# Kernel tuning notes

Measured on AMD Instinct MI355X. Metric: run time of the kernel, lower is better.

## Reference

```python
import jax, jax.numpy as jnp
import numpy as np
from jax import lax

B, S, T = 2048, 4096, 3


def setup_inputs() -> dict:
    key = jax.random.key(0)
    k_em, k_tr, k_st, k_en, k_tg = jax.random.split(key, 5)
    emissions = jax.random.normal(k_em, (B, S, T), dtype=jnp.float32)
    # reset_parameters(): uniform(-0.1, 0.1)
    transitions = jax.random.uniform(k_tr, (T, T), minval=-0.1, maxval=0.1, dtype=jnp.float32)
    start_transitions = jax.random.uniform(k_st, (T,), minval=-0.1, maxval=0.1, dtype=jnp.float32)
    end_transitions = jax.random.uniform(k_en, (T,), minval=-0.1, maxval=0.1, dtype=jnp.float32)
    tags = jax.random.randint(k_tg, (B, S), 0, T, dtype=jnp.int32)
    mask = jnp.ones((B, S), dtype=jnp.int32)
    return {
        "emissions": emissions,
        "transitions": transitions,
        "start_transitions": start_transitions,
        "end_transitions": end_transitions,
        "tags": tags,
        "mask": mask,
    }


def _crf_nll(emissions, transitions, start_transitions, end_transitions, tags, mask):
    # batch_first=True -> transpose to time-major (S, B, ...)
    em = jnp.transpose(emissions, (1, 0, 2))  # (S, B, T)
    tg = jnp.transpose(tags, (1, 0))          # (S, B)
    mk = jnp.transpose(mask, (1, 0))          # (S, B)
    batch_idx = jnp.arange(em.shape[1])

    # ---- log partition (forward algorithm) ----
    alpha0 = start_transitions[None, :] + em[0]  # (B, T)

    def fwd_step(alpha, inp):
        e, m = inp  # e: (B,T), m: (B,)
        # alpha[b,i] + trans[i,j] + e[b,j] -> logsumexp over i
        nxt = jax.nn.logsumexp(alpha[:, :, None] + transitions[None, :, :] + e[:, None, :], axis=1)
        alpha = jnp.where((m > 0)[:, None], nxt, alpha)
        return alpha, None

    alpha, _ = lax.scan(fwd_step, alpha0, (em[1:], mk[1:]))
    log_partition = jax.nn.logsumexp(alpha + end_transitions[None, :], axis=1)  # (B,)

    # ---- gold score ----
    score0 = start_transitions[tg[0]] + em[0][batch_idx, tg[0]]  # (B,)

    def score_step(carry, inp):
        score, prev = carry
        e, t, m = inp
        add = transitions[prev, t] + e[batch_idx, t]
        score = score + jnp.where(m > 0, add, jnp.zeros_like(score))
        return (score, t), None

    (score, _), _ = lax.scan(score_step, (score0, tg[0]), (em[1:], tg[1:], mk[1:]))
    seq_lens = jnp.sum(mk, axis=0)  # (B,)
    last_tags = tg[seq_lens - 1, batch_idx]
    score = score + end_transitions[last_tags]

    return jnp.mean(log_partition - score)


def reference(emissions, transitions, start_transitions, end_transitions, tags, mask):
    return _crf_nll(emissions, transitions, start_transitions, end_transitions, tags, mask)
```

## Files before the change

kernel.cpp:

```cpp
#include <hip/hip_runtime.h>
#include <math.h>

#define CRF_B 2048
#define CRF_S 4096
#define LN2F  0.6931471805599453f

__device__ __forceinline__ float fexp2(float x) { return __builtin_amdgcn_exp2f(x); }

#define CRF_MERGE(aq0,aq1,aq2,aq3,aq4,aq5,aq6,aq7,aq8,aC0,aC1,aC2,asc,acn, \
                  bq0,bq1,bq2,bq3,bq4,bq5,bq6,bq7,bq8,bC0,bC1,bC2,bsc,bcn) { \
    int cm_ = max(max(bC0,bC1),bC2);                                        \
    int d0_=bC0-cm_, d1_=bC1-cm_, d2_=bC2-cm_;                              \
    float s0_ = (d0_>-127)? __int_as_float((127+d0_)<<23) : 0.f;            \
    float s1_ = (d1_>-127)? __int_as_float((127+d1_)<<23) : 0.f;            \
    float s2_ = (d2_>-127)? __int_as_float((127+d2_)<<23) : 0.f;            \
    float b0_=bq0*s0_, b1_=bq1*s0_, b2_=bq2*s0_;                            \
    float b3_=bq3*s1_, b4_=bq4*s1_, b5_=bq5*s1_;                            \
    float b6_=bq6*s2_, b7_=bq7*s2_, b8_=bq8*s2_;                            \
    float r0_=aq0*b0_+aq1*b3_+aq2*b6_;                                      \
    float r1_=aq0*b1_+aq1*b4_+aq2*b7_;                                      \
    float r2_=aq0*b2_+aq1*b5_+aq2*b8_;                                      \
    float r3_=aq3*b0_+aq4*b3_+aq5*b6_;                                      \
    float r4_=aq3*b1_+aq4*b4_+aq5*b7_;                                      \
    float r5_=aq3*b2_+aq4*b5_+aq5*b8_;                                      \
    float r6_=aq6*b0_+aq7*b3_+aq8*b6_;                                      \
    float r7_=aq6*b1_+aq7*b4_+aq8*b7_;                                      \
    float r8_=aq6*b2_+aq7*b5_+aq8*b8_;                                      \
    float mx_; int ex_; float sc_;                                          \
    mx_=fmaxf(fmaxf(r0_,r1_),r2_); ex_=((__float_as_int(mx_)>>23)&255)-127; \
    sc_=__int_as_float((127-ex_)<<23);                                      \
    aq0=r0_*sc_; aq1=r1_*sc_; aq2=r2_*sc_; aC0=aC0+cm_+ex_;                 \
    mx_=fmaxf(fmaxf(r3_,r4_),r5_); ex_=((__float_as_int(mx_)>>23)&255)-127; \
    sc_=__int_as_float((127-ex_)<<23);                                      \
    aq3=r3_*sc_; aq4=r4_*sc_; aq5=r5_*sc_; aC1=aC1+cm_+ex_;                 \
    mx_=fmaxf(fmaxf(r6_,r7_),r8_); ex_=((__float_as_int(mx_)>>23)&255)-127; \
    sc_=__int_as_float((127-ex_)<<23);                                      \
    aq6=r6_*sc_; aq7=r7_*sc_; aq8=r8_*sc_; aC2=aC2+cm_+ex_;                 \
    asc += bsc; acn += bcn; }

__global__ __launch_bounds__(512, 6) void crf_row_kernel(
    const float* __restrict__ em,
    const float* __restrict__ trans,
    const float* __restrict__ startt,
    const float* __restrict__ endt,
    const int*   __restrict__ tags,
    const int*   __restrict__ mask,
    float* __restrict__ perb)
{
    __shared__ float s_tr[9];
    __shared__ float s_rq[8][10];
    __shared__ int   s_rc[8][4];

    const int tid = threadIdx.x;
    const int w = tid >> 6, l = tid & 63;
    const int b = blockIdx.x;
    const long cbase = (long)b * CRF_S + (long)tid * 8;

    if (tid < 9) s_tr[tid] = trans[tid];
    __syncthreads();

    const float4* e4 = (const float4*)(em + cbase * 3);
    float4 ev0 = e4[0], ev1 = e4[1], ev2 = e4[2],
           ev3 = e4[3], ev4 = e4[4], ev5 = e4[5];
    const int4* t4 = (const int4*)(tags + cbase);
    int4 ta = t4[0], tb = t4[1];
    const int4* m4 = (const int4*)(mask + cbase);
    int4 ma = m4[0], mb = m4[1];
    int p = 0;
    if (tid > 0) p = tags[cbase - 1];

    float e[24] = { ev0.x, ev0.y, ev0.z, ev0.w, ev1.x, ev1.y, ev1.z, ev1.w,
                    ev2.x, ev2.y, ev2.z, ev2.w, ev3.x, ev3.y, ev3.z, ev3.w,
                    ev4.x, ev4.y, ev4.z, ev4.w, ev5.x, ev5.y, ev5.z, ev5.w };
    unsigned ttag =  (unsigned)(ta.x & 3)        | ((unsigned)(ta.y & 3) << 2)
                  | ((unsigned)(ta.z & 3) << 4)  | ((unsigned)(ta.w & 3) << 6)
                  | ((unsigned)(tb.x & 3) << 8)  | ((unsigned)(tb.y & 3) << 10)
                  | ((unsigned)(tb.z & 3) << 12) | ((unsigned)(tb.w & 3) << 14);
    unsigned tmsk =  (unsigned)(ma.x != 0)       | ((unsigned)(ma.y != 0) << 1)
                  | ((unsigned)(ma.z != 0) << 2) | ((unsigned)(ma.w != 0) << 3)
                  | ((unsigned)(mb.x != 0) << 4) | ((unsigned)(mb.y != 0) << 5)
                  | ((unsigned)(mb.z != 0) << 6) | ((unsigned)(mb.w != 0) << 7);

    float Etr[9];
    #pragma unroll
    for (int k = 0; k < 9; ++k) Etr[k] = __expf(s_tr[k]);

    float q0=1.f,q1=0.f,q2=0.f, q3=0.f,q4=1.f,q5=0.f, q6=0.f,q7=0.f,q8=1.f;
    int C0=0, C1=0, C2=0;
    float score = 0.f; int cnt = 0;

    #pragma unroll
    for (int t = 0; t < 8; ++t) {
        float e0 = e[3*t], e1 = e[3*t+1], e2 = e[3*t+2];
        int tv = (int)((ttag >> (2*t)) & 3u);
        int mv = (int)((tmsk >> t) & 1u);
        if (mv && !((t == 0) && (tid == 0))) {
            float X0 = __expf(e0), X1 = __expf(e1), X2 = __expf(e2);
            float n0, n1, n2;
            n0 = q0*Etr[0] + q1*Etr[3] + q2*Etr[6];
            n1 = q0*Etr[1] + q1*Etr[4] + q2*Etr[7];
            n2 = q0*Etr[2] + q1*Etr[5] + q2*Etr[8];
            q0 = n0*X0; q1 = n1*X1; q2 = n2*X2;
            n0 = q3*Etr[0] + q4*Etr[3] + q5*Etr[6];
            n1 = q3*Etr[1] + q4*Etr[4] + q5*Etr[7];
            n2 = q3*Etr[2] + q4*Etr[5] + q5*Etr[8];
            q3 = n0*X0; q4 = n1*X1; q5 = n2*X2;
            n0 = q6*Etr[0] + q7*Etr[3] + q8*Etr[6];
            n1 = q6*Etr[1] + q7*Etr[4] + q8*Etr[7];
            n2 = q6*Etr[2] + q7*Etr[5] + q8*Etr[8];
            q6 = n0*X0; q7 = n1*X1; q8 = n2*X2;
            float ev = (tv == 0) ? e0 : (tv == 1) ? e1 : e2;
            score += s_tr[p * 3 + tv] + ev;
            ++cnt;
        }
        p = tv;
        if ((t & 3) == 3) {
            float mx; int ex; float sc;
            mx = fmaxf(fmaxf(q0, q1), q2);
            ex = ((__float_as_int(mx) >> 23) & 255) - 127;
            sc = __int_as_float((127 - ex) << 23);
            q0 *= sc; q1 *= sc; q2 *= sc; C0 += ex;
            mx = fmaxf(fmaxf(q3, q4), q5);
            ex = ((__float_as_int(mx) >> 23) & 255) - 127;
            sc = __int_as_float((127 - ex) << 23);
            q3 *= sc; q4 *= sc; q5 *= sc; C1 += ex;
            mx = fmaxf(fmaxf(q6, q7), q8);
            ex = ((__float_as_int(mx) >> 23) & 255) - 127;
            sc = __int_as_float((127 - ex) << 23);
            q6 *= sc; q7 *= sc; q8 *= sc; C2 += ex;
        }
    }

    #pragma unroll
    for (int st = 1; st < 64; st <<= 1) {
        float nq0 = __shfl_down(q0, st), nq1 = __shfl_down(q1, st),
              nq2 = __shfl_down(q2, st), nq3 = __shfl_down(q3, st),
              nq4 = __shfl_down(q4, st), nq5 = __shfl_down(q5, st),
              nq6 = __shfl_down(q6, st), nq7 = __shfl_down(q7, st),
              nq8 = __shfl_down(q8, st);
        int nC0 = __shfl_down(C0, st), nC1 = __shfl_down(C1, st),
            nC2 = __shfl_down(C2, st);
        float nsc = __shfl_down(score, st);
        int   ncn = __shfl_down(cnt, st);
        CRF_MERGE(q0,q1,q2,q3,q4,q5,q6,q7,q8,C0,C1,C2,score,cnt,
                  nq0,nq1,nq2,nq3,nq4,nq5,nq6,nq7,nq8,nC0,nC1,nC2,nsc,ncn);
    }

    if (l == 0) {
        s_rq[w][0]=q0; s_rq[w][1]=q1; s_rq[w][2]=q2;
        s_rq[w][3]=q3; s_rq[w][4]=q4; s_rq[w][5]=q5;
        s_rq[w][6]=q6; s_rq[w][7]=q7; s_rq[w][8]=q8;
        s_rq[w][9]=score;
        s_rc[w][0]=C0; s_rc[w][1]=C1; s_rc[w][2]=C2; s_rc[w][3]=cnt;
    }
    __syncthreads();

    if (tid == 0) {
        float a0=s_rq[0][0], a1=s_rq[0][1], a2=s_rq[0][2],
              a3=s_rq[0][3], a4=s_rq[0][4], a5=s_rq[0][5],
              a6=s_rq[0][6], a7=s_rq[0][7], a8=s_rq[0][8];
        float asc = s_rq[0][9];
        int AC0=s_rc[0][0], AC1=s_rc[0][1], AC2=s_rc[0][2], acn=s_rc[0][3];
        #pragma unroll
        for (int w2 = 1; w2 < 8; ++w2) {
            float m0=s_rq[w2][0], m1=s_rq[w2][1], m2=s_rq[w2][2],
                  m3=s_rq[w2][3], m4=s_rq[w2][4], m5=s_rq[w2][5],
                  m6=s_rq[w2][6], m7=s_rq[w2][7], m8=s_rq[w2][8];
            float msc = s_rq[w2][9];
            int mc0=s_rc[w2][0], mc1=s_rc[w2][1], mc2=s_rc[w2][2], mcn=s_rc[w2][3];
            CRF_MERGE(a0,a1,a2,a3,a4,a5,a6,a7,a8,AC0,AC1,AC2,asc,acn,
                      m0,m1,m2,m3,m4,m5,m6,m7,m8,mc0,mc1,mc2,msc,mcn);
        }
        int tg0 = (int)(ttag & 3u), mk0 = (int)(tmsk & 1u);
        float la0 = startt[0] + e[0];
        float la1 = startt[1] + e[1];
        float la2 = startt[2] + e[2];
        float am = fmaxf(fmaxf(la0, la1), la2);
        int cm = max(max(AC0, AC1), AC2);
        float w0 = __expf(la0 - am) * fexp2((float)(AC0 - cm));
        float w1 = __expf(la1 - am) * fexp2((float)(AC1 - cm));
        float w2v = __expf(la2 - am) * fexp2((float)(AC2 - cm));
        float v0 = w0*a0 + w1*a3 + w2v*a6;
        float v1 = w0*a1 + w1*a4 + w2v*a7;
        float v2 = w0*a2 + w1*a5 + w2v*a8;
        float sum = v0 * __expf(endt[0]) + v1 * __expf(endt[1])
                  + v2 * __expf(endt[2]);
        float lp = am + (float)cm * LN2F + __logf(sum);

        float sc = asc + startt[tg0]
                 + ((tg0 == 0) ? e[0] : (tg0 == 1) ? e[1] : e[2]);
        int cn = acn + mk0;
        int lastidx = (cn > 0) ? (cn - 1) : 0;
        sc += endt[tags[(long)b * CRF_S + lastidx]];

        perb[b] = lp - sc;
    }
}

__global__ __launch_bounds__(256) void crf_reduce_kernel(
    const float* __restrict__ perb, float* __restrict__ out)
{
    __shared__ float sdata[256];
    const int tid = threadIdx.x;
    float s = 0.f;
    for (int i = tid; i < CRF_B; i += 256) s += perb[i];
    sdata[tid] = s;
    __syncthreads();
    for (int off = 128; off > 0; off >>= 1) {
        if (tid < off) sdata[tid] += sdata[tid + off];
        __syncthreads();
    }
    if (tid == 0) out[0] = sdata[0] * (1.0f / (float)CRF_B);
}

extern "C" void kernel_launch(void* const* d_in, const int* in_sizes, int n_in,
                              void* d_out, int out_size, void* d_ws, size_t ws_size,
                              hipStream_t stream)
{
    const float* em     = (const float*)d_in[0];
    const float* trans  = (const float*)d_in[1];
    const float* startt = (const float*)d_in[2];
    const float* endt   = (const float*)d_in[3];
    const int*   tags   = (const int*)d_in[4];
    const int*   mask   = (const int*)d_in[5];
    float* out = (float*)d_out;

    float* perb = (float*)d_ws;

    crf_row_kernel<<<CRF_B, 512, 0, stream>>>(
        em, trans, startt, endt, tags, mask, perb);
    crf_reduce_kernel<<<1, 256, 0, stream>>>(perb, out);
}
```

Baseline: 45.10 us.

## Use single shared scale exponent per matrix and double per-thread sequence chunk

Each thread now processes 16 timesteps instead of 8 with 256-thread blocks, halving the depth of the cross-wave merge work. The per-row exponent tracking of the 3x3 transfer matrices is collapsed into one shared scale exponent per matrix, which simplifies the merge macro (no per-row rescale) and the final combine. Thread 0 also reuses its own registers instead of rereading shared memory. The single exponent risks underflow of small rows when row magnitudes diverge, though with small transitions this is benign; higher register use may reduce occupancy.

Measured after the change: 59.11 us. 31.1% more time.

```diff
diff --git a/kernel.cpp b/kernel.cpp
--- a/kernel.cpp
+++ b/kernel.cpp
@@ -5,40 +5,29 @@
 #define CRF_S 4096
 #define LN2F  0.6931471805599453f
 
-__device__ __forceinline__ float fexp2(float x) { return __builtin_amdgcn_exp2f(x); }
-
-#define CRF_MERGE(aq0,aq1,aq2,aq3,aq4,aq5,aq6,aq7,aq8,aC0,aC1,aC2,asc,acn, \
-                  bq0,bq1,bq2,bq3,bq4,bq5,bq6,bq7,bq8,bC0,bC1,bC2,bsc,bcn) { \
-    int cm_ = max(max(bC0,bC1),bC2);                                        \
-    int d0_=bC0-cm_, d1_=bC1-cm_, d2_=bC2-cm_;                              \
-    float s0_ = (d0_>-127)? __int_as_float((127+d0_)<<23) : 0.f;            \
-    float s1_ = (d1_>-127)? __int_as_float((127+d1_)<<23) : 0.f;            \
-    float s2_ = (d2_>-127)? __int_as_float((127+d2_)<<23) : 0.f;            \
-    float b0_=bq0*s0_, b1_=bq1*s0_, b2_=bq2*s0_;                            \
-    float b3_=bq3*s1_, b4_=bq4*s1_, b5_=bq5*s1_;                            \
-    float b6_=bq6*s2_, b7_=bq7*s2_, b8_=bq8*s2_;                            \
-    float r0_=aq0*b0_+aq1*b3_+aq2*b6_;                                      \
-    float r1_=aq0*b1_+aq1*b4_+aq2*b7_;                                      \
-    float r2_=aq0*b2_+aq1*b5_+aq2*b8_;                                      \
-    float r3_=aq3*b0_+aq4*b3_+aq5*b6_;                                      \
-    float r4_=aq3*b1_+aq4*b4_+aq5*b7_;                                      \
-    float r5_=aq3*b2_+aq4*b5_+aq5*b8_;                                      \
-    float r6_=aq6*b0_+aq7*b3_+aq8*b6_;                                      \
-    float r7_=aq6*b1_+aq7*b4_+aq8*b7_;                                      \
-    float r8_=aq6*b2_+aq7*b5_+aq8*b8_;                                      \
-    float mx_; int ex_; float sc_;                                          \
-    mx_=fmaxf(fmaxf(r0_,r1_),r2_); ex_=((__float_as_int(mx_)>>23)&255)-127; \
-    sc_=__int_as_float((127-ex_)<<23);                                      \
-    aq0=r0_*sc_; aq1=r1_*sc_; aq2=r2_*sc_; aC0=aC0+cm_+ex_;                 \
-    mx_=fmaxf(fmaxf(r3_,r4_),r5_); ex_=((__float_as_int(mx_)>>23)&255)-127; \
-    sc_=__int_as_float((127-ex_)<<23);                                      \
-    aq3=r3_*sc_; aq4=r4_*sc_; aq5=r5_*sc_; aC1=aC1+cm_+ex_;                 \
-    mx_=fmaxf(fmaxf(r6_,r7_),r8_); ex_=((__float_as_int(mx_)>>23)&255)-127; \
-    sc_=__int_as_float((127-ex_)<<23);                                      \
-    aq6=r6_*sc_; aq7=r7_*sc_; aq8=r8_*sc_; aC2=aC2+cm_+ex_;                 \
+#define CRF_MERGE(aq0,aq1,aq2,aq3,aq4,aq5,aq6,aq7,aq8,aC,asc,acn, \
+                  bq0,bq1,bq2,bq3,bq4,bq5,bq6,bq7,bq8,bC,bsc,bcn) { \
+    float r0_=aq0*bq0+aq1*bq3+aq2*bq6;                              \
+    float r1_=aq0*bq1+aq1*bq4+aq2*bq7;                              \
+    float r2_=aq0*bq2+aq1*bq5+aq2*bq8;                              \
+    float r3_=aq3*bq0+aq4*bq3+aq5*bq6;                              \
+    float r4_=aq3*bq1+aq4*bq4+aq5*bq7;                              \
+    float r5_=aq3*bq2+aq4*bq5+aq5*bq8;                              \
+    float r6_=aq6*bq0+aq7*bq3+aq8*bq6;                              \
+    float r7_=aq6*bq1+aq7*bq4+aq8*bq7;                              \
+    float r8_=aq6*bq2+aq7*bq5+aq8*bq8;                              \
+    float mx_ = fmaxf(fmaxf(fmaxf(fmaxf(r0_,r1_),r2_),              \
+                            fmaxf(fmaxf(r3_,r4_),r5_)),             \
+                      fmaxf(fmaxf(r6_,r7_),r8_));                   \
+    int ex_ = ((__float_as_int(mx_)>>23)&255)-127;                  \
+    float sc_ = __int_as_float((127-ex_)<<23);                      \
+    aq0=r0_*sc_; aq1=r1_*sc_; aq2=r2_*sc_;                          \
+    aq3=r3_*sc_; aq4=r4_*sc_; aq5=r5_*sc_;                          \
+    aq6=r6_*sc_; aq7=r7_*sc_; aq8=r8_*sc_;                          \
+    aC = aC + bC + ex_;                                             \
     asc += bsc; acn += bcn; }
 
-__global__ __launch_bounds__(512, 6) void crf_row_kernel(
+__global__ __launch_bounds__(256, 5) void crf_row_kernel(
     const float* __restrict__ em,
     const float* __restrict__ trans,
     const float* __restrict__ startt,
@@ -48,49 +37,59 @@
     float* __restrict__ perb)
 {
     __shared__ float s_tr[9];
-    __shared__ float s_rq[8][10];
-    __shared__ int   s_rc[8][4];
+    __shared__ float s_rq[4][10];
+    __shared__ int   s_rc[4][2];
 
     const int tid = threadIdx.x;
     const int w = tid >> 6, l = tid & 63;
     const int b = blockIdx.x;
-    const long cbase = (long)b * CRF_S + (long)tid * 8;
+    const long cbase = (long)b * CRF_S + (long)tid * 16;
 
     if (tid < 9) s_tr[tid] = trans[tid];
     __syncthreads();
 
-    const float4* e4 = (const float4*)(em + cbase * 3);
-    float4 ev0 = e4[0], ev1 = e4[1], ev2 = e4[2],
-           ev3 = e4[3], ev4 = e4[4], ev5 = e4[5];
     const int4* t4 = (const int4*)(tags + cbase);
-    int4 ta = t4[0], tb = t4[1];
+    int4 ta = t4[0], tb = t4[1], tc = t4[2], td = t4[3];
     const int4* m4 = (const int4*)(mask + cbase);
-    int4 ma = m4[0], mb = m4[1];
+    int4 ma = m4[0], mb = m4[1], mc = m4[2], md = m4[3];
     int p = 0;
     if (tid > 0) p = tags[cbase - 1];
 
-    float e[24] = { ev0.x, ev0.y, ev0.z, ev0.w, ev1.x, ev1.y, ev1.z, ev1.w,
-                    ev2.x, ev2.y, ev2.z, ev2.w, ev3.x, ev3.y, ev3.z, ev3.w,
-                    ev4.x, ev4.y, ev4.z, ev4.w, ev5.x, ev5.y, ev5.z, ev5.w };
     unsigned ttag =  (unsigned)(ta.x & 3)        | ((unsigned)(ta.y & 3) << 2)
                   | ((unsigned)(ta.z & 3) << 4)  | ((unsigned)(ta.w & 3) << 6)
                   | ((unsigned)(tb.x & 3) << 8)  | ((unsigned)(tb.y & 3) << 10)
-                  | ((unsigned)(tb.z & 3) << 12) | ((unsigned)(tb.w & 3) << 14);
-    unsigned tmsk =  (unsigned)(ma.x != 0)       | ((unsigned)(ma.y != 0) << 1)
-                  | ((unsigned)(ma.z != 0) << 2) | ((unsigned)(ma.w != 0) << 3)
-                  | ((unsigned)(mb.x != 0) << 4) | ((unsigned)(mb.y != 0) << 5)
-                  | ((unsigned)(mb.z != 0) << 6) | ((unsigned)(mb.w != 0) << 7);
+                  | ((unsigned)(tb.z & 3) << 12) | ((unsigned)(tb.w & 3) << 14)
+                  | ((unsigned)(tc.x & 3) << 16) | ((unsigned)(tc.y & 3) << 18)
+                  | ((unsigned)(tc.z & 3) << 20) | ((unsigned)(tc.w & 3) << 22)
+                  | ((unsigned)(td.x & 3) << 24) | ((unsigned)(td.y & 3) << 26)
+                  | ((unsigned)(td.z & 3) << 28) | ((unsigned)(td.w & 3) << 30);
+    unsigned tmsk =  (unsigned)(ma.x != 0)        | ((unsigned)(ma.y != 0) << 1)
+                  | ((unsigned)(ma.z != 0) << 2)  | ((unsigned)(ma.w != 0) << 3)
+                  | ((unsigned)(mb.x != 0) << 4)  | ((unsigned)(mb.y != 0) << 5)
+                  | ((unsigned)(mb.z != 0) << 6)  | ((unsigned)(mb.w != 0) << 7)
+                  | ((unsigned)(mc.x != 0) << 8)  | ((unsigned)(mc.y != 0) << 9)
+                  | ((unsigned)(mc.z != 0) << 10) | ((unsigned)(mc.w != 0) << 11)
+                  | ((unsigned)(md.x != 0) << 12) | ((unsigned)(md.y != 0) << 13)
+                  | ((unsigned)(md.z != 0) << 14) | ((unsigned)(md.w != 0) << 15);
+
+    const float4* e4 = (const float4*)(em + cbase * 3);
+    float e[48];
+    #pragma unroll
+    for (int k = 0; k < 12; ++k) {
+        float4 v = e4[k];
+        e[4*k+0] = v.x; e[4*k+1] = v.y; e[4*k+2] = v.z; e[4*k+3] = v.w;
+    }
 
     float Etr[9];
     #pragma unroll
     for (int k = 0; k < 9; ++k) Etr[k] = __expf(s_tr[k]);
 
     float q0=1.f,q1=0.f,q2=0.f, q3=0.f,q4=1.f,q5=0.f, q6=0.f,q7=0.f,q8=1.f;
-    int C0=0, C1=0, C2=0;
+    int C = 0;
     float score = 0.f; int cnt = 0;
 
     #pragma unroll
-    for (int t = 0; t < 8; ++t) {
+    for (int t = 0; t < 16; ++t) {
         float e0 = e[3*t], e1 = e[3*t+1], e2 = e[3*t+2];
         int tv = (int)((ttag >> (2*t)) & 3u);
         int mv = (int)((tmsk >> t) & 1u);
@@ -115,19 +114,15 @@
         }
         p = tv;
         if ((t & 3) == 3) {
-            float mx; int ex; float sc;
-            mx = fmaxf(fmaxf(q0, q1), q2);
-            ex = ((__float_as_int(mx) >> 23) & 255) - 127;
-            sc = __int_as_float((127 - ex) << 23);
-            q0 *= sc; q1 *= sc; q2 *= sc; C0 += ex;
-            mx = fmaxf(fmaxf(q3, q4), q5);
-            ex = ((__float_as_int(mx) >> 23) & 255) - 127;
-            sc = __int_as_float((127 - ex) << 23);
-            q3 *= sc; q4 *= sc; q5 *= sc; C1 += ex;
-            mx = fmaxf(fmaxf(q6, q7), q8);
-            ex = ((__float_as_int(mx) >> 23) & 255) - 127;
-            sc = __int_as_float((127 - ex) << 23);
-            q6 *= sc; q7 *= sc; q8 *= sc; C2 += ex;
+            float mx = fmaxf(fmaxf(fmaxf(fmaxf(q0,q1),q2),
+                                   fmaxf(fmaxf(q3,q4),q5)),
+                             fmaxf(fmaxf(q6,q7),q8));
+            int ex = ((__float_as_int(mx) >> 23) & 255) - 127;
+            float sc = __int_as_float((127 - ex) << 23);
+            q0 *= sc; q1 *= sc; q2 *= sc;
+            q3 *= sc; q4 *= sc; q5 *= sc;
+            q6 *= sc; q7 *= sc; q8 *= sc;
+            C += ex;
         }
     }
 
@@ -138,12 +133,11 @@
               nq4 = __shfl_down(q4, st), nq5 = __shfl_down(q5, st),
               nq6 = __shfl_down(q6, st), nq7 = __shfl_down(q7, st),
               nq8 = __shfl_down(q8, st);
-        int nC0 = __shfl_down(C0, st), nC1 = __shfl_down(C1, st),
-            nC2 = __shfl_down(C2, st);
+        int   nC  = __shfl_down(C, st);
         float nsc = __shfl_down(score, st);
         int   ncn = __shfl_down(cnt, st);
-        CRF_MERGE(q0,q1,q2,q3,q4,q5,q6,q7,q8,C0,C1,C2,score,cnt,
-                  nq0,nq1,nq2,nq3,nq4,nq5,nq6,nq7,nq8,nC0,nC1,nC2,nsc,ncn);
+        CRF_MERGE(q0,q1,q2,q3,q4,q5,q6,q7,q8,C,score,cnt,
+                  nq0,nq1,nq2,nq3,nq4,nq5,nq6,nq7,nq8,nC,nsc,ncn);
     }
 
     if (l == 0) {
@@ -151,41 +145,38 @@
         s_rq[w][3]=q3; s_rq[w][4]=q4; s_rq[w][5]=q5;
         s_rq[w][6]=q6; s_rq[w][7]=q7; s_rq[w][8]=q8;
         s_rq[w][9]=score;
-        s_rc[w][0]=C0; s_rc[w][1]=C1; s_rc[w][2]=C2; s_rc[w][3]=cnt;
+        s_rc[w][0]=C;  s_rc[w][1]=cnt;
     }
     __syncthreads();
 
     if (tid == 0) {
-        float a0=s_rq[0][0], a1=s_rq[0][1], a2=s_rq[0][2],
-              a3=s_rq[0][3], a4=s_rq[0][4], a5=s_rq[0][5],
-              a6=s_rq[0][6], a7=s_rq[0][7], a8=s_rq[0][8];
-        float asc = s_rq[0][9];
-        int AC0=s_rc[0][0], AC1=s_rc[0][1], AC2=s_rc[0][2], acn=s_rc[0][3];
+        float a0=q0, a1=q1, a2=q2, a3=q3, a4=q4, a5=q5, a6=q6, a7=q7, a8=q8;
+        float asc = score;
+        int AC = C, acn = cnt;
         #pragma unroll
-        for (int w2 = 1; w2 < 8; ++w2) {
+        for (int w2 = 1; w2 < 4; ++w2) {
             float m0=s_rq[w2][0], m1=s_rq[w2][1], m2=s_rq[w2][2],
                   m3=s_rq[w2][3], m4=s_rq[w2][4], m5=s_rq[w2][5],
                   m6=s_rq[w2][6], m7=s_rq[w2][7], m8=s_rq[w2][8];
             float msc = s_rq[w2][9];
-            int mc0=s_rc[w2][0], mc1=s_rc[w2][1], mc2=s_rc[w2][2], mcn=s_rc[w2][3];
-            CRF_MERGE(a0,a1,a2,a3,a4,a5,a6,a7,a8,AC0,AC1,AC2,asc,acn,
-                      m0,m1,m2,m3,m4,m5,m6,m7,m8,mc0,mc1,mc2,msc,mcn);
+            int mC = s_rc[w2][0], mcn = s_rc[w2][1];
+            CRF_MERGE(a0,a1,a2,a3,a4,a5,a6,a7,a8,AC,asc,acn,
+                      m0,m1,m2,m3,m4,m5,m6,m7,m8,mC,msc,mcn);
         }
         int tg0 = (int)(ttag & 3u), mk0 = (int)(tmsk & 1u);
         float la0 = startt[0] + e[0];
         float la1 = startt[1] + e[1];
         float la2 = startt[2] + e[2];
         float am = fmaxf(fmaxf(la0, la1), la2);
-        int cm = max(max(AC0, AC1), AC2);
-        float w0 = __expf(la0 - am) * fexp2((float)(AC0 - cm));
-        float w1 = __expf(la1 - am) * fexp2((float)(AC1 - cm));
-        float w2v = __expf(la2 - am) * fexp2((float)(AC2 - cm));
+        float w0  = __expf(la0 - am);
+        float w1  = __expf(la1 - am);
+        float w2v = __expf(la2 - am);
         float v0 = w0*a0 + w1*a3 + w2v*a6;
         float v1 = w0*a1 + w1*a4 + w2v*a7;
         float v2 = w0*a2 + w1*a5 + w2v*a8;
         float sum = v0 * __expf(endt[0]) + v1 * __expf(endt[1])
                   + v2 * __expf(endt[2]);
-        float lp = am + (float)cm * LN2F + __logf(sum);
+        float lp = am + (float)AC * LN2F + __logf(sum);
 
         float sc = asc + startt[tg0]
                  + ((tg0 == 0) ? e[0] : (tg0 == 1) ? e[1] : e[2]);
@@ -227,7 +218,7 @@
 
     float* perb = (float*)d_ws;
 
-    crf_row_kernel<<<CRF_B, 512, 0, stream>>>(
+    crf_row_kernel<<<CRF_B, 256, 0, stream>>>(
         em, trans, startt, endt, tags, mask, perb);
     crf_reduce_kernel<<<1, 256, 0, stream>>>(perb, out);
 }
```
